# Optimization experiments

Hardware: AMD Instinct MI355X
Metric: run time of the kernel (lower is better)

The kernel has to match this reference:

```python
import jax, jax.numpy as jnp
import numpy as np

B, T, C, H = 8, 2048, 1024, 128


def setup_inputs() -> dict:
    key = jax.random.key(0)
    k1, k2, k3, k4 = jax.random.split(key, 4)
    x = jax.random.normal(k1, (B, T, C), dtype=jnp.float32)
    # torch nn.Linear(n_embed, head_size, bias=False) weights, stored as [C, H] for x @ W
    scale = 1.0 / np.sqrt(C)
    Wk = jax.random.normal(k2, (C, H), dtype=jnp.float32) * scale
    Wq = jax.random.normal(k3, (C, H), dtype=jnp.float32) * scale
    Wv = jax.random.normal(k4, (C, H), dtype=jnp.float32) * scale
    return {"x": x, "Wk": Wk, "Wq": Wq, "Wv": Wv}


def reference(x, Wk, Wq, Wv):
    # Faithful translation of Head.forward (dropout = identity in eval mode).
    Bx, Tx, Cx = x.shape
    k = x @ Wk  # [B,T,H]
    q = x @ Wq  # [B,T,H]
    v = x @ Wv  # [B,T,H]
    # NOTE: original scales by C**-0.5 (n_embed), not head_size**-0.5.
    scores = jnp.einsum('bth,bsh->bts', q, k) * (Cx ** -0.5)  # [B,T,T]
    causal = jnp.tril(jnp.ones((Tx, Tx), dtype=bool))  # tril buffer
    scores = jnp.where(causal, scores, -jnp.inf)
    weights = jax.nn.softmax(scores, axis=-1)
    out = jnp.einsum('bts,bsh->bth', weights, v)  # [B,T,H]
    return out
```

## Files before the change

### kernel.cpp

```cpp
#include <hip/hip_runtime.h>
#include <type_traits>

#define Bn 8
#define Tn 2048
#define Cn 1024
#define Hn 128
#define Mn (Bn*Tn)

typedef __attribute__((ext_vector_type(4))) float f32x4;
typedef __attribute__((ext_vector_type(2))) float f32x2;
typedef __attribute__((ext_vector_type(16))) float f32x16;
typedef __attribute__((ext_vector_type(8))) short s16x8;
typedef __attribute__((ext_vector_type(4))) int i32x4;
typedef __attribute__((ext_vector_type(2))) int i32x2;
typedef unsigned int u32;

__device__ __forceinline__ unsigned short f2bf(float f) {
  union { float f; unsigned u; } v; v.f = f;
  unsigned r = v.u + 0x7FFFu + ((v.u >> 16) & 1u);
  return (unsigned short)(r >> 16);
}

__device__ __forceinline__ float bf2f(unsigned s) {
  return __builtin_bit_cast(float, s << 16);
}

__device__ __forceinline__ unsigned cvtpk(float lo, float hi) {
  unsigned r;
  asm("v_cvt_pk_bf16_f32 %0, %1, %2" : "=v"(r) : "v"(lo), "v"(hi));
  return r;
}

__device__ __forceinline__ i32x2 swap32(int a, int b) {
#if __has_builtin(__builtin_amdgcn_permlane32_swap)
  return __builtin_amdgcn_permlane32_swap(a, b, false, false);
#else
  int ax = __shfl_xor(a, 32), bx = __shfl_xor(b, 32);
  i32x2 r;
  r[0] = (threadIdx.x & 32) ? bx : a;
  r[1] = (threadIdx.x & 32) ? b : ax;
  return r;
#endif
}

__device__ __forceinline__ void gl_lds16(const void* g, void* l) {
  __builtin_amdgcn_global_load_lds((const __attribute__((address_space(1))) u32*)g,
                                   (__attribute__((address_space(3))) u32*)l, 16, 0, 0);
}

__global__ __launch_bounds__(256) void prep_wt(const float* __restrict__ Wq,
                                               const float* __restrict__ Wk,
                                               const float* __restrict__ Wv,
                                               unsigned short* __restrict__ Wt) {
  __shared__ float tile[64][33];
  const int w = blockIdx.z;
  const float* W = (w == 0) ? Wq : (w == 1) ? Wk : Wv;
  const float scale = (w == 0) ? 0.03125f : 1.0f;
  const int c0 = blockIdx.x * 64, h0 = blockIdx.y * 32;
  const int tid = threadIdx.x;
  const int hl = tid & 31, cg = tid >> 5;
#pragma unroll
  for (int i = 0; i < 8; i++) {
    int cl = cg * 8 + i;
    tile[cl][hl] = W[(c0 + cl) * Hn + h0 + hl];
  }
  __syncthreads();
  const int cl2 = tid & 63, hg = tid >> 6;
#pragma unroll
  for (int i = 0; i < 8; i++) {
    int hl2 = hg * 8 + i;
    Wt[(size_t)(w * Hn + h0 + hl2) * Cn + c0 + cl2] = f2bf(tile[cl2][hl2] * scale);
  }
}

__global__ __launch_bounds__(512, 1) void proj_fused(const float* __restrict__ x,
                                                     const unsigned short* __restrict__ Wt,
                                                     unsigned short* __restrict__ qkv) {
  __shared__ __align__(16) unsigned short Abuf[2][64 * 64];
  __shared__ __align__(16) unsigned short Bbuf[2][384 * 64];
  const int tid = threadIdx.x;
  const int lane = tid & 63, wv = tid >> 6;
  const int wm = wv >> 2, wn = wv & 3;
  const int l31 = lane & 31, hi = lane >> 5;
  const int bm = blockIdx.x * 64;
  const int phase = (blockIdx.x >> 3) & 15;

  const int ar = tid >> 3;
  const int as = tid & 7;

  f32x16 acc[3];
#pragma unroll
  for (int i = 0; i < 3; i++)
#pragma unroll
    for (int r = 0; r < 16; r++) acc[i][r] = 0.f;

  auto slice = [&](int u) { return ((u + phase) & 15) * 64; };

  auto stageB = [&](int buf, int kk) {
#pragma unroll
    for (int i = 0; i < 6; i++) {
      int r0 = wv * 48 + i * 8;
      int n = r0 + (lane >> 3);
      const unsigned short* src = Wt + (size_t)n * Cn + kk + (((lane & 7) ^ (n & 7)) << 3);
      gl_lds16(src, &Bbuf[buf][r0 * 64]);
    }
  };
  auto loadA = [&](int kk, float4& v0, float4& v1) {
    const float* g = x + (size_t)(bm + ar) * Cn + kk + as * 8;
    v0 = *(const float4*)g;
    v1 = *(const float4*)(g + 4);
  };
  auto writeA = [&](int buf, float4 v0, float4 v1) {
    i32x4 w = {(int)cvtpk(v0.x, v0.y), (int)cvtpk(v0.z, v0.w),
               (int)cvtpk(v1.x, v1.y), (int)cvtpk(v1.z, v1.w)};
    *(i32x4*)&Abuf[buf][ar * 64 + ((as ^ (ar & 7)) << 3)] = w;
  };

  {
    float4 a0, a1;
    loadA(slice(0), a0, a1);
    stageB(0, slice(0));
    writeA(0, a0, a1);
  }

  const int arow = wm * 32 + l31;

  auto body = [&](int u, auto PC) {
    constexpr int P = decltype(PC)::value;
    const bool more = (u < 15);
    float4 a0, a1;
    if (more) loadA(slice(u + 1), a0, a1);
    __builtin_amdgcn_s_barrier();
    if (more) {
      stageB(P ^ 1, slice(u + 1));
      asm volatile("s_waitcnt vmcnt(8) lgkmcnt(0)" ::: "memory");
    } else {
      asm volatile("s_waitcnt vmcnt(0) lgkmcnt(0)" ::: "memory");
    }
    __builtin_amdgcn_s_barrier();
    __builtin_amdgcn_sched_barrier(0);
    s16x8 aF[4];
#pragma unroll
    for (int ks = 0; ks < 4; ks++)
      aF[ks] = *(const s16x8*)&Abuf[P][arow * 64 + (((ks * 2 + hi) ^ (arow & 7)) << 3)];
    __builtin_amdgcn_s_setprio(1);
#pragma unroll
    for (int ks = 0; ks < 4; ks++)
#pragma unroll
      for (int ni = 0; ni < 3; ni++) {
        int brow = wn * 96 + ni * 32 + l31;
        s16x8 bF = *(const s16x8*)&Bbuf[P][brow * 64 + (((ks * 2 + hi) ^ (brow & 7)) << 3)];
        acc[ni] = __builtin_amdgcn_mfma_f32_32x32x16_bf16(aF[ks], bF, acc[ni], 0, 0, 0);
      }
    __builtin_amdgcn_s_setprio(0);
    if (more) writeA(P ^ 1, a0, a1);
  };

  for (int u = 0; u < 16; u += 2) {
    body(u, std::integral_constant<int, 0>{});
    body(u + 1, std::integral_constant<int, 1>{});
  }

#pragma unroll
  for (int ni = 0; ni < 3; ni++) {
    const int cb = wn * 3 + ni;
    if (cb < 8) {
      const int w = cb >> 2;
      const int h = (cb & 3) * 32 + l31;
      unsigned short* o = qkv + (size_t)w * ((size_t)Mn * Hn);
#pragma unroll
      for (int r = 0; r < 16; r++) {
        int m = bm + wm * 32 + (r & 3) + 8 * (r >> 2) + 4 * hi;
        o[(size_t)m * Hn + h] = f2bf(acc[ni][r]);
      }
    } else {
      const int h = (cb - 8) * 32 + l31;
      const int bb = bm >> 11;
      const int tl0 = (bm & 2047) + wm * 32;
      unsigned short* vt = qkv + (size_t)2 * Mn * Hn + (size_t)bb * (Hn * Tn) + (size_t)h * Tn;
#pragma unroll
      for (int r = 0; r < 16; r++)
        vt[tl0 + (r & 3) + 8 * (r >> 2) + 4 * hi] = f2bf(acc[ni][r]);
    }
  }
}

__global__ __launch_bounds__(256, 2) void attn_fwd(const unsigned short* __restrict__ qkv,
                                                   unsigned short* __restrict__ o_part,
                                                   float* __restrict__ ml,
                                                   int sshift) {
  __shared__ __align__(16) unsigned short Kl[2][64 * 128];
  __shared__ __align__(16) unsigned short Vl[2][128 * 64];

  const int bid = blockIdx.x;
  const int b = bid & 7;
  const int r = bid >> 3;
  const int jj = r & 15;
  const int sp = r >> 4;
  const int S = 1 << sshift;
  const int j = (S > 1 && sp >= (S >> 1)) ? (15 - jj) : jj;
  const int s = sp;

  const int tid = threadIdx.x;
  const int lane = tid & 63, wv = tid >> 6;
  const int l31 = lane & 31, hi = lane >> 5;

  const unsigned short* qb  = qkv + (size_t)b * (Tn * Hn);
  const unsigned short* kb  = qkv + (size_t)(Mn * Hn) + (size_t)b * (Tn * Hn);
  const unsigned short* vtb = qkv + (size_t)2 * (Mn * Hn) + (size_t)b * (Hn * Tn);

  const int qrow0 = j * 128 + wv * 32;
  const int qg = qrow0 + l31;

  const int ntt = (j + 1) * 2;
  const int tlo = (s * ntt) >> sshift;
  const int thi = ((s + 1) * ntt) >> sshift;

  f32x16 oT[4];
#pragma unroll
  for (int i = 0; i < 4; i++)
#pragma unroll
    for (int q = 0; q < 16; q++) oT[i][q] = 0.f;
  float m_ = -1e30f, l_ = 0.f;

  auto stage = [&](int buf, int tile) {
    const int kvb0 = tile * 64;
#pragma unroll
    for (int i = 0; i < 4; i++) {
      int r0 = wv * 16 + i * 4;
      int row = r0 + (lane >> 4);
      int ch = lane & 15;
      const unsigned short* src = kb + (size_t)(kvb0 + row) * Hn + ((ch ^ (row & 7)) << 3);
      gl_lds16(src, &Kl[buf][r0 * 128]);
    }
#pragma unroll
    for (int i = 0; i < 4; i++) {
      int r0 = wv * 32 + i * 8;
      int row = r0 + (lane >> 3);
      int ch = lane & 7;
      const unsigned short* src = vtb + (size_t)row * Tn + kvb0 + ((ch ^ (row & 7)) << 3);
      gl_lds16(src, &Vl[buf][r0 * 64]);
    }
  };

  if (tlo < thi) {
    s16x8 qB[8];
#pragma unroll
    for (int hs = 0; hs < 8; hs++)
      qB[hs] = *(const s16x8*)(qb + (size_t)qg * Hn + hs * 16 + hi * 8);

    stage(0, tlo);
    int buf = 0;

    for (int t = tlo; t < thi; t++) {
      if (t + 1 < thi) {
        stage(buf ^ 1, t + 1);
        asm volatile("s_waitcnt vmcnt(8)" ::: "memory");
      } else {
        asm volatile("s_waitcnt vmcnt(0)" ::: "memory");
      }
      __builtin_amdgcn_s_barrier();
      __builtin_amdgcn_sched_barrier(0);
      const int kvb = t * 64;
      if (kvb < qrow0 + 32) {
        const unsigned short* Kb = &Kl[buf][0];
        f32x16 sv0, sv1;
#pragma unroll
        for (int q = 0; q < 16; q++) { sv0[q] = 0.f; sv1[q] = 0.f; }
        __builtin_amdgcn_s_setprio(1);
        {
          const int row = l31;
#pragma unroll
          for (int hs = 0; hs < 8; hs++) {
            s16x8 kf = *(const s16x8*)&Kb[row * 128 + (((hs * 2 + hi) ^ (row & 7)) << 3)];
            sv0 = __builtin_amdgcn_mfma_f32_32x32x16_bf16(kf, qB[hs], sv0, 0, 0, 0);
          }
        }
        {
          const int row = 32 + l31;
#pragma unroll
          for (int hs = 0; hs < 8; hs++) {
            s16x8 kf = *(const s16x8*)&Kb[row * 128 + (((hs * 2 + hi) ^ (row & 7)) << 3)];
            sv1 = __builtin_amdgcn_mfma_f32_32x32x16_bf16(kf, qB[hs], sv1, 0, 0, 0);
          }
        }
        __builtin_amdgcn_s_setprio(0);
        if (kvb + 63 > qrow0) {
#pragma unroll
          for (int q = 0; q < 16; q++) {
            int kr = (q & 3) + 8 * (q >> 2) + 4 * hi;
            if (kvb + kr > qg) sv0[q] = -1e30f;
            if (kvb + 32 + kr > qg) sv1[q] = -1e30f;
          }
        }
        float om = sv0[0];
#pragma unroll
        for (int q = 1; q < 16; q++) om = fmaxf(om, sv0[q]);
#pragma unroll
        for (int q = 0; q < 16; q++) om = fmaxf(om, sv1[q]);
        i32x2 mx = swap32(__builtin_bit_cast(int, om), __builtin_bit_cast(int, om));
        float pm = __builtin_bit_cast(float, hi ? mx[0] : mx[1]);
        float tmax = fmaxf(om, pm);
        if (__any(tmax > m_ + 8.f)) {
          float mn = fmaxf(m_, tmax);
          float sc = __expf(m_ - mn);
          m_ = mn; l_ *= sc;
#pragma unroll
          for (int i = 0; i < 4; i++)
#pragma unroll
            for (int q = 0; q < 16; q++) oT[i][q] *= sc;
        }
        float osum = 0.f;
#pragma unroll
        for (int q = 0; q < 16; q++) { sv0[q] = __expf(sv0[q] - m_); osum += sv0[q]; }
#pragma unroll
        for (int q = 0; q < 16; q++) { sv1[q] = __expf(sv1[q] - m_); osum += sv1[q]; }
        i32x2 sx = swap32(__builtin_bit_cast(int, osum), __builtin_bit_cast(int, osum));
        float psum = __builtin_bit_cast(float, hi ? sx[0] : sx[1]);
        l_ += osum + psum;
        s16x8 pB[4];
        {
          unsigned PK[8];
#pragma unroll
          for (int n = 0; n < 8; n++) PK[n] = cvtpk(sv0[2 * n], sv0[2 * n + 1]);
          i32x2 e0 = swap32((int)PK[0], (int)PK[2]);
          i32x2 e1 = swap32((int)PK[1], (int)PK[3]);
          i32x2 e2 = swap32((int)PK[4], (int)PK[6]);
          i32x2 e3 = swap32((int)PK[5], (int)PK[7]);
          i32x4 w0 = {e0[0], e1[0], e0[1], e1[1]};
          i32x4 w1 = {e2[0], e3[0], e2[1], e3[1]};
          pB[0] = __builtin_bit_cast(s16x8, w0);
          pB[1] = __builtin_bit_cast(s16x8, w1);
        }
        {
          unsigned PK[8];
#pragma unroll
          for (int n = 0; n < 8; n++) PK[n] = cvtpk(sv1[2 * n], sv1[2 * n + 1]);
          i32x2 e0 = swap32((int)PK[0], (int)PK[2]);
          i32x2 e1 = swap32((int)PK[1], (int)PK[3]);
          i32x2 e2 = swap32((int)PK[4], (int)PK[6]);
          i32x2 e3 = swap32((int)PK[5], (int)PK[7]);
          i32x4 w0 = {e0[0], e1[0], e0[1], e1[1]};
          i32x4 w1 = {e2[0], e3[0], e2[1], e3[1]};
          pB[2] = __builtin_bit_cast(s16x8, w0);
          pB[3] = __builtin_bit_cast(s16x8, w1);
        }
        __builtin_amdgcn_s_setprio(1);
#pragma unroll
        for (int hsl = 0; hsl < 4; hsl++) {
          const int row = hsl * 32 + l31;
#pragma unroll
          for (int ks = 0; ks < 4; ks++) {
            s16x8 vf = *(const s16x8*)&Vl[buf][row * 64 + (((ks * 2 + hi) ^ (row & 7)) << 3)];
            oT[hsl] = __builtin_amdgcn_mfma_f32_32x32x16_bf16(vf, pB[ks], oT[hsl], 0, 0, 0);
          }
        }
        __builtin_amdgcn_s_setprio(0);
      }
      __builtin_amdgcn_s_barrier();
      buf ^= 1;
    }
  }

  unsigned short* orow = o_part + (size_t)s * ((size_t)Mn * Hn) + (size_t)(b * Tn + qg) * Hn;
#pragma unroll
  for (int hsl = 0; hsl < 4; hsl++)
#pragma unroll
    for (int g = 0; g < 4; g++) {
      unsigned p0 = cvtpk(oT[hsl][4 * g + 0], oT[hsl][4 * g + 1]);
      unsigned p1 = cvtpk(oT[hsl][4 * g + 2], oT[hsl][4 * g + 3]);
      i32x2 st = {(int)p0, (int)p1};
      *(i32x2*)(orow + hsl * 32 + g * 8 + hi * 4) = st;
    }
  if (lane < 32) {
    f32x2 w = {m_, l_};
    *(f32x2*)(ml + (size_t)s * (Mn * 2) + (size_t)(b * Tn + qg) * 2) = w;
  }
}

__global__ __launch_bounds__(256) void combine(const unsigned short* __restrict__ o_part,
                                               const float* __restrict__ ml,
                                               float* __restrict__ out, int S) {
  const int q = blockIdx.x * 4 + (threadIdx.x >> 6);
  const int p = threadIdx.x & 63;
  float M = -1e30f;
  for (int s = 0; s < S; s++) M = fmaxf(M, ml[(size_t)s * (Mn * 2) + q * 2]);
  float L = 0.f, a0 = 0.f, a1 = 0.f;
  for (int s = 0; s < S; s++) {
    float ms = ml[(size_t)s * (Mn * 2) + q * 2];
    float ls = ml[(size_t)s * (Mn * 2) + q * 2 + 1];
    float w = __expf(ms - M);
    L += ls * w;
    u32 v = *(const u32*)(o_part + (size_t)s * ((size_t)Mn * Hn) + (size_t)q * Hn + p * 2);
    a0 += bf2f(v & 0xffffu) * w;
    a1 += bf2f(v >> 16) * w;
  }
  float2 o = {a0 / L, a1 / L};
  *(float2*)(out + (size_t)q * Hn + p * 2) = o;
}

extern "C" void kernel_launch(void* const* d_in, const int* in_sizes, int n_in,
                              void* d_out, int out_size, void* d_ws, size_t ws_size,
                              hipStream_t stream) {
  const float* x  = (const float*)d_in[0];
  const float* Wk = (const float*)d_in[1];
  const float* Wq = (const float*)d_in[2];
  const float* Wv = (const float*)d_in[3];
  float* out = (float*)d_out;

  char* ws = (char*)d_ws;
  const size_t wt_b  = 786432;
  const size_t qkv_b = (size_t)3 * Mn * Hn * 2;
  const size_t base  = wt_b + qkv_b;
  const size_t per   = (size_t)Mn * Hn * 2 + (size_t)Mn * 8;
  int sshift = (ws_size >= base + 4 * per) ? 2 : (ws_size >= base + 2 * per) ? 1 : 0;
  const int S = 1 << sshift;

  unsigned short* Wt  = (unsigned short*)ws;
  unsigned short* qkv = (unsigned short*)(ws + wt_b);
  unsigned short* o_part = (unsigned short*)(ws + base);
  float* mlp = (float*)(ws + base + (size_t)S * Mn * Hn * 2);

  prep_wt<<<dim3(16, 4, 3), 256, 0, stream>>>(Wq, Wk, Wv, Wt);
  proj_fused<<<256, 512, 0, stream>>>(x, Wt, qkv);
  attn_fwd<<<128 * S, 256, 0, stream>>>(qkv, o_part, mlp, sshift);
  combine<<<Mn / 4, 256, 0, stream>>>(o_part, mlp, out, S);
}
```

Baseline: 63.63 us.

## Retile QKV projection to 128x192 blocks with 2D grid and 256 threads

The projection GEMM changes from 64-row blocks computing all 384 output columns with 512 threads to 128-row blocks computing 192 columns with 256 threads over a 128x2 grid. Each wave now computes a 64x96 tile with two M sub-tiles, raising MFMA work per B fragment load and allowing two blocks per CU. In exchange, each row of x is fetched by two blocks, doubling global reads of the fp32 input unless the cache absorbs them.

```diff
diff --git a/kernel.cpp b/kernel.cpp
--- a/kernel.cpp
+++ b/kernel.cpp
@@ -73,26 +73,29 @@
   }
 }
 
-__global__ __launch_bounds__(512, 1) void proj_fused(const float* __restrict__ x,
+__global__ __launch_bounds__(256, 2) void proj_fused(const float* __restrict__ x,
                                                      const unsigned short* __restrict__ Wt,
                                                      unsigned short* __restrict__ qkv) {
-  __shared__ __align__(16) unsigned short Abuf[2][64 * 64];
-  __shared__ __align__(16) unsigned short Bbuf[2][384 * 64];
+  __shared__ __align__(16) unsigned short Abuf[2][128 * 64];
+  __shared__ __align__(16) unsigned short Bbuf[2][192 * 64];
   const int tid = threadIdx.x;
   const int lane = tid & 63, wv = tid >> 6;
-  const int wm = wv >> 2, wn = wv & 3;
+  const int wm = wv >> 1, wn = wv & 1;
   const int l31 = lane & 31, hi = lane >> 5;
-  const int bm = blockIdx.x * 64;
+  const int bm = blockIdx.x * 128;
+  const int bn = blockIdx.y * 192;
   const int phase = (blockIdx.x >> 3) & 15;
 
   const int ar = tid >> 3;
   const int as = tid & 7;
 
-  f32x16 acc[3];
-#pragma unroll
-  for (int i = 0; i < 3; i++)
-#pragma unroll
-    for (int r = 0; r < 16; r++) acc[i][r] = 0.f;
+  f32x16 acc[2][3];
+#pragma unroll
+  for (int mi = 0; mi < 2; mi++)
+#pragma unroll
+    for (int ni = 0; ni < 3; ni++)
+#pragma unroll
+      for (int r = 0; r < 16; r++) acc[mi][ni][r] = 0.f;
 
   auto slice = [&](int u) { return ((u + phase) & 15) * 64; };
 
@@ -101,59 +104,72 @@
     for (int i = 0; i < 6; i++) {
       int r0 = wv * 48 + i * 8;
       int n = r0 + (lane >> 3);
-      const unsigned short* src = Wt + (size_t)n * Cn + kk + (((lane & 7) ^ (n & 7)) << 3);
+      const unsigned short* src = Wt + (size_t)(bn + n) * Cn + kk +
+                                  (((lane & 7) ^ (n & 7)) << 3);
       gl_lds16(src, &Bbuf[buf][r0 * 64]);
     }
   };
-  auto loadA = [&](int kk, float4& v0, float4& v1) {
-    const float* g = x + (size_t)(bm + ar) * Cn + kk + as * 8;
-    v0 = *(const float4*)g;
-    v1 = *(const float4*)(g + 4);
+  auto loadA = [&](int kk, float4* R) {
+#pragma unroll
+    for (int i = 0; i < 4; i++) {
+      const float* g = x + (size_t)(bm + ar + i * 32) * Cn + kk + as * 8;
+      R[2 * i]     = *(const float4*)g;
+      R[2 * i + 1] = *(const float4*)(g + 4);
+    }
   };
-  auto writeA = [&](int buf, float4 v0, float4 v1) {
-    i32x4 w = {(int)cvtpk(v0.x, v0.y), (int)cvtpk(v0.z, v0.w),
-               (int)cvtpk(v1.x, v1.y), (int)cvtpk(v1.z, v1.w)};
-    *(i32x4*)&Abuf[buf][ar * 64 + ((as ^ (ar & 7)) << 3)] = w;
+  auto writeA = [&](int buf, const float4* R) {
+#pragma unroll
+    for (int i = 0; i < 4; i++) {
+      int row = ar + i * 32;
+      i32x4 w = {(int)cvtpk(R[2 * i].x, R[2 * i].y),
+                 (int)cvtpk(R[2 * i].z, R[2 * i].w),
+                 (int)cvtpk(R[2 * i + 1].x, R[2 * i + 1].y),
+                 (int)cvtpk(R[2 * i + 1].z, R[2 * i + 1].w)};
+      *(i32x4*)&Abuf[buf][row * 64 + ((as ^ (row & 7)) << 3)] = w;
+    }
   };
 
   {
-    float4 a0, a1;
-    loadA(slice(0), a0, a1);
+    float4 R[8];
+    loadA(slice(0), R);
     stageB(0, slice(0));
-    writeA(0, a0, a1);
-  }
-
-  const int arow = wm * 32 + l31;
+    writeA(0, R);
+  }
 
   auto body = [&](int u, auto PC) {
     constexpr int P = decltype(PC)::value;
     const bool more = (u < 15);
-    float4 a0, a1;
-    if (more) loadA(slice(u + 1), a0, a1);
+    float4 R[8];
+    if (more) loadA(slice(u + 1), R);
     __builtin_amdgcn_s_barrier();
     if (more) {
       stageB(P ^ 1, slice(u + 1));
-      asm volatile("s_waitcnt vmcnt(8) lgkmcnt(0)" ::: "memory");
+      asm volatile("s_waitcnt vmcnt(14) lgkmcnt(0)" ::: "memory");
     } else {
       asm volatile("s_waitcnt vmcnt(0) lgkmcnt(0)" ::: "memory");
     }
     __builtin_amdgcn_s_barrier();
     __builtin_amdgcn_sched_barrier(0);
-    s16x8 aF[4];
+    s16x8 aF[2][4];
+#pragma unroll
+    for (int mi = 0; mi < 2; mi++) {
+      const int arow = wm * 64 + mi * 32 + l31;
+#pragma unroll
+      for (int ks = 0; ks < 4; ks++)
+        aF[mi][ks] = *(const s16x8*)&Abuf[P][arow * 64 + (((ks * 2 + hi) ^ (arow & 7)) << 3)];
+    }
+    __builtin_amdgcn_s_setprio(1);
 #pragma unroll
     for (int ks = 0; ks < 4; ks++)
-      aF[ks] = *(const s16x8*)&Abuf[P][arow * 64 + (((ks * 2 + hi) ^ (arow & 7)) << 3)];
-    __builtin_amdgcn_s_setprio(1);
-#pragma unroll
-    for (int ks = 0; ks < 4; ks++)
 #pragma unroll
       for (int ni = 0; ni < 3; ni++) {
-        int brow = wn * 96 + ni * 32 + l31;
+        const int brow = wn * 96 + ni * 32 + l31;
         s16x8 bF = *(const s16x8*)&Bbuf[P][brow * 64 + (((ks * 2 + hi) ^ (brow & 7)) << 3)];
-        acc[ni] = __builtin_amdgcn_mfma_f32_32x32x16_bf16(aF[ks], bF, acc[ni], 0, 0, 0);
+        acc[0][ni] = __builtin_amdgcn_mfma_f32_32x32x16_bf16(aF[0][ks], bF, acc[0][ni], 0, 0, 0);
+        acc[1][ni] = __builtin_amdgcn_mfma_f32_32x32x16_bf16(aF[1][ks], bF, acc[1][ni], 0, 0, 0);
       }
     __builtin_amdgcn_s_setprio(0);
-    if (more) writeA(P ^ 1, a0, a1);
+    if (more) writeA(P ^ 1, R);
   };
 
   for (int u = 0; u < 16; u += 2) {
@@ -162,27 +178,29 @@
   }
 
 #pragma unroll
-  for (int ni = 0; ni < 3; ni++) {
-    const int cb = wn * 3 + ni;
-    if (cb < 8) {
-      const int w = cb >> 2;
-      const int h = (cb & 3) * 32 + l31;
-      unsigned short* o = qkv + (size_t)w * ((size_t)Mn * Hn);
-#pragma unroll
-      for (int r = 0; r < 16; r++) {
-        int m = bm + wm * 32 + (r & 3) + 8 * (r >> 2) + 4 * hi;
-        o[(size_t)m * Hn + h] = f2bf(acc[ni][r]);
+  for (int mi = 0; mi < 2; mi++)
+#pragma unroll
+    for (int ni = 0; ni < 3; ni++) {
+      const int cb = blockIdx.y * 6 + wn * 3 + ni;
+      if (cb < 8) {
+        const int w = cb >> 2;
+        const int h = (cb & 3) * 32 + l31;
+        unsigned short* o = qkv + (size_t)w * ((size_t)Mn * Hn);
+#pragma unroll
+        for (int r = 0; r < 16; r++) {
+          int m = bm + wm * 64 + mi * 32 + (r & 3) + 8 * (r >> 2) + 4 * hi;
+          o[(size_t)m * Hn + h] = f2bf(acc[mi][ni][r]);
+        }
+      } else {
+        const int h = (cb - 8) * 32 + l31;
+        const int bb = bm >> 11;
+        const int tl0 = (bm & 2047) + wm * 64 + mi * 32;
+        unsigned short* vt = qkv + (size_t)2 * Mn * Hn + (size_t)bb * (Hn * Tn) + (size_t)h * Tn;
+#pragma unroll
+        for (int r = 0; r < 16; r++)
+          vt[tl0 + (r & 3) + 8 * (r >> 2) + 4 * hi] = f2bf(acc[mi][ni][r]);
       }
-    } else {
-      const int h = (cb - 8) * 32 + l31;
-      const int bb = bm >> 11;
-      const int tl0 = (bm & 2047) + wm * 32;
-      unsigned short* vt = qkv + (size_t)2 * Mn * Hn + (size_t)bb * (Hn * Tn) + (size_t)h * Tn;
-#pragma unroll
-      for (int r = 0; r < 16; r++)
-        vt[tl0 + (r & 3) + 8 * (r >> 2) + 4 * hi] = f2bf(acc[ni][r]);
-    }
-  }
+    }
 }
 
 __global__ __launch_bounds__(256, 2) void attn_fwd(const unsigned short* __restrict__ qkv,
@@ -422,7 +440,7 @@
   float* mlp = (float*)(ws + base + (size_t)S * Mn * Hn * 2);
 
   prep_wt<<<dim3(16, 4, 3), 256, 0, stream>>>(Wq, Wk, Wv, Wt);
-  proj_fused<<<256, 512, 0, stream>>>(x, Wt, qkv);
+  proj_fused<<<dim3(128, 2), 256, 0, stream>>>(x, Wt, qkv);
   attn_fwd<<<128 * S, 256, 0, stream>>>(qkv, o_part, mlp, sshift);
   combine<<<Mn / 4, 256, 0, stream>>>(o_part, mlp, out, S);
 }
```

New measurement: 67.40 us. 1.06x slower.
